# Optimization experiments

Hardware: AMD Instinct MI355X
Metric: run time of the kernel (lower is better)

Reference implementation:

```python
import jax, jax.numpy as jnp
import numpy as np

B, LQ, LK = 4, 256, 512
DQ = DK = PROJ = 256


def setup_inputs() -> dict:
    key = jax.random.key(0)
    ks = jax.random.split(key, 8)
    query = jax.random.normal(ks[0], (B, LQ, DQ), dtype=jnp.float32)
    keys = jax.random.normal(ks[1], (B, LK, DK), dtype=jnp.float32)
    attn_mask = jax.random.bernoulli(ks[2], 0.1, (B, LQ, LK))
    # Linear(query_size+key_size, proj) split into query/key halves (same math as concat @ W1)
    s1 = 1.0 / np.sqrt(DQ + DK)
    Wq = jax.random.uniform(ks[3], (DQ, PROJ), jnp.float32, -s1, s1)
    Wk = jax.random.uniform(ks[4], (DK, PROJ), jnp.float32, -s1, s1)
    b1 = jax.random.uniform(ks[5], (PROJ,), jnp.float32, -s1, s1)
    s2 = 1.0 / np.sqrt(PROJ)
    w2 = jax.random.uniform(ks[6], (PROJ,), jnp.float32, -s2, s2)
    b2 = jax.random.uniform(ks[7], (), jnp.float32, -s2, s2)
    return {"query": query, "keys": keys, "attn_mask": attn_mask,
            "Wq": Wq, "Wk": Wk, "b1": b1, "w2": w2, "b2": b2}


def reference(query, keys, attn_mask, Wq, Wk, b1, w2, b2):
    # cat(q_expand, k_expand) @ W1 == q@Wq broadcast-added to k@Wk (avoids the huge concat)
    qp = jnp.einsum('bqd,dp->bqp', query, Wq)            # (B,Lq,P)
    kp = jnp.einsum('bkd,dp->bkp', keys, Wk)             # (B,Lk,P)
    h = jnp.tanh(qp[:, :, None, :] + kp[:, None, :, :] + b1)  # (B,Lq,Lk,P)
    logits = jnp.einsum('bqkp,p->bqk', h, w2) + b2        # (B,Lq,Lk)
    logits = jnp.where(attn_mask, -jnp.inf, logits)
    return logits
```

## Files before the change

### kernel.cpp

```cpp
#include <hip/hip_runtime.h>
#include <math.h>

#define B_ 4
#define LQ_ 256
#define LK_ 512
#define D_ 256
#define P_ 256

#define SC 2.8853900817779268f

#define MASK_SENTINEL (-3.0e38f)

__global__ __launch_bounds__(128) void proj_kernel(
    const float* __restrict__ Q, const float* __restrict__ Kx,
    const float* __restrict__ Wq, const float* __restrict__ Wk,
    const float* __restrict__ b1,
    float* __restrict__ Eq, float* __restrict__ Ek)
{
    __shared__ __align__(16) float As[64][36];
    __shared__ __align__(16) float Ws[64][68];

    const int bm = blockIdx.x >> 2;
    const int bn = blockIdx.x & 3;
    const bool isq = (bm < 32);
    const int m0 = isq ? bm * 32 : (bm - 32) * 32;
    const float* A = isq ? Q : Kx;
    const float* W = isq ? Wq : Wk;
    float* outp    = isq ? Eq : Ek;
    const int n0 = bn * 64;

    const int t  = threadIdx.x;
    const int tx = t & 15;
    const int ty = t >> 4;

    float acc[4][4] = {};

    for (int kt = 0; kt < 4; ++kt) {
        const int d0 = kt * 64;
        __syncthreads();
        #pragma unroll
        for (int i = 0; i < 4; ++i) {
            int f  = t + i * 128;
            int m  = f >> 4;
            int c4 = (f & 15) * 4;
            float4 v = *(const float4*)&A[(size_t)(m0 + m) * D_ + d0 + c4];
            As[c4 + 0][m] = v.x;
            As[c4 + 1][m] = v.y;
            As[c4 + 2][m] = v.z;
            As[c4 + 3][m] = v.w;
        }
        #pragma unroll
        for (int i = 0; i < 8; ++i) {
            int f  = t + i * 128;
            int r  = f >> 4;
            int c4 = (f & 15) * 4;
            *(float4*)&Ws[r][c4] = *(const float4*)&W[(size_t)(d0 + r) * P_ + n0 + c4];
        }
        __syncthreads();
        #pragma unroll 8
        for (int k = 0; k < 64; ++k) {
            float4 a = *(const float4*)&As[k][ty * 4];
            float4 w = *(const float4*)&Ws[k][tx * 4];
            float av[4] = {a.x, a.y, a.z, a.w};
            float wv[4] = {w.x, w.y, w.z, w.w};
            #pragma unroll
            for (int i = 0; i < 4; ++i)
                #pragma unroll
                for (int j = 0; j < 4; ++j)
                    acc[i][j] = fmaf(av[i], wv[j], acc[i][j]);
        }
    }

    float bv[4] = {0.f, 0.f, 0.f, 0.f};
    if (!isq) {
        float4 b = *(const float4*)&b1[n0 + tx * 4];
        bv[0] = b.x; bv[1] = b.y; bv[2] = b.z; bv[3] = b.w;
    }

    #pragma unroll
    for (int i = 0; i < 4; ++i) {
        int m = m0 + ty * 4 + i;
        float4 o;
        o.x = __builtin_amdgcn_exp2f(SC * (acc[i][0] + bv[0]));
        o.y = __builtin_amdgcn_exp2f(SC * (acc[i][1] + bv[1]));
        o.z = __builtin_amdgcn_exp2f(SC * (acc[i][2] + bv[2]));
        o.w = __builtin_amdgcn_exp2f(SC * (acc[i][3] + bv[3]));
        *(float4*)&outp[(size_t)m * P_ + n0 + tx * 4] = o;
    }
}

__global__ __launch_bounds__(256) void logits_kernel(
    const float* __restrict__ Eq, const float* __restrict__ Ek,
    const unsigned char* __restrict__ mask,
    const float* __restrict__ w2, const float* __restrict__ b2,
    float* __restrict__ out)
{
    __shared__ __align__(16) float eqs[32][260];
    __shared__ __align__(16) float eks[32][260];
    __shared__ __align__(16) float ws2[256];
    __shared__ float partial[4];

    const int b  = blockIdx.z;
    const int q0 = blockIdx.y * 32;
    const int k0 = blockIdx.x * 32;
    const int t  = threadIdx.x;

    #pragma unroll
    for (int i = 0; i < 8; ++i) {
        int f = t + i * 256;
        int r = f >> 6;
        int c = (f & 63) * 4;
        *(float4*)&eqs[r][c] = *(const float4*)&Eq[(size_t)(b * LQ_ + q0 + r) * P_ + c];
        *(float4*)&eks[r][c] = *(const float4*)&Ek[(size_t)(b * LK_ + k0 + r) * P_ + c];
    }
    float wv = w2[t];
    ws2[t] = wv;
    #pragma unroll
    for (int s = 32; s > 0; s >>= 1) wv += __shfl_xor(wv, s);
    if ((t & 63) == 0) partial[t >> 6] = wv;
    __syncthreads();

    const float base = partial[0] + partial[1] + partial[2] + partial[3] + b2[0];

    const int tx = t & 15;
    const int ty = t >> 4;

    size_t oidx[2][2];
    unsigned char mb[2][2];
    #pragma unroll
    for (int i = 0; i < 2; ++i)
        #pragma unroll
        for (int j = 0; j < 2; ++j) {
            oidx[i][j] = (size_t)(b * LQ_ + q0 + ty + i * 16) * LK_ + (k0 + tx + j * 16);
            mb[i][j] = mask[oidx[i][j]];
        }

    const float* q0p = &eqs[ty][0];
    const float* q1p = &eqs[ty + 16][0];
    const float* k0p = &eks[tx][0];
    const float* k1p = &eks[tx + 16][0];

    float acc[2][2] = {};

    #pragma unroll 4
    for (int p4 = 0; p4 < 64; ++p4) {
        float4 qv[2], kv[2], w;
        qv[0] = *(const float4*)(q0p + p4 * 4);
        qv[1] = *(const float4*)(q1p + p4 * 4);
        kv[0] = *(const float4*)(k0p + p4 * 4);
        kv[1] = *(const float4*)(k1p + p4 * 4);
        w     = *(const float4*)&ws2[p4 * 4];
        float qa[2][4] = {{qv[0].x,qv[0].y,qv[0].z,qv[0].w},
                          {qv[1].x,qv[1].y,qv[1].z,qv[1].w}};
        float ka[2][4] = {{kv[0].x,kv[0].y,kv[0].z,kv[0].w},
                          {kv[1].x,kv[1].y,kv[1].z,kv[1].w}};
        #pragma unroll
        for (int i = 0; i < 2; ++i)
            #pragma unroll
            for (int j = 0; j < 2; ++j) {
                float x0 = fmaf(qa[i][0], ka[j][0], 1.f);
                float x1 = fmaf(qa[i][1], ka[j][1], 1.f);
                float x2 = fmaf(qa[i][2], ka[j][2], 1.f);
                float x3 = fmaf(qa[i][3], ka[j][3], 1.f);
                float d01 = x0 * x1;
                float d23 = x2 * x3;
                float n01 = fmaf(w.x, x1, w.y * x0);
                float n23 = fmaf(w.z, x3, w.w * x2);
                float den = d01 * d23;
                float num = fmaf(n01, d23, n23 * d01);
                acc[i][j] = fmaf(num, __builtin_amdgcn_rcpf(den), acc[i][j]);
            }
    }

    #pragma unroll
    for (int i = 0; i < 2; ++i)
        #pragma unroll
        for (int j = 0; j < 2; ++j)
            out[oidx[i][j]] = mb[i][j] ? MASK_SENTINEL : fmaf(-2.f, acc[i][j], base);
}

extern "C" void kernel_launch(void* const* d_in, const int* in_sizes, int n_in,
                              void* d_out, int out_size, void* d_ws, size_t ws_size,
                              hipStream_t stream) {
    const float* query        = (const float*)d_in[0];
    const float* keys         = (const float*)d_in[1];
    const unsigned char* mask = (const unsigned char*)d_in[2];
    const float* Wq           = (const float*)d_in[3];
    const float* Wk           = (const float*)d_in[4];
    const float* b1           = (const float*)d_in[5];
    const float* w2           = (const float*)d_in[6];
    const float* b2           = (const float*)d_in[7];
    float* out = (float*)d_out;

    float* Eq = (float*)d_ws;
    float* Ek = Eq + (size_t)B_ * LQ_ * P_;

    proj_kernel<<<384, 128, 0, stream>>>(query, keys, Wq, Wk, b1, Eq, Ek);

    dim3 g2(LK_ / 32, LQ_ / 32, B_);
    logits_kernel<<<g2, 256, 0, stream>>>(Eq, Ek, mask, w2, b2, out);
}
```

Baseline: 37.54 us.

## Split logits over P into partial tiles with 4x4 register blocking plus combine kernel

The logits kernel now uses 64x64 q/k tiles with a 4x4 per-thread register block and splits the P dimension into four 64-wide chunks across blocks, writing partial sums to a workspace. A new combine kernel sums the four partials, applies bias and mask with vectorized float4 loads and stores, and writes the output. The aim is more reuse of each shared-memory load and a smaller shared-memory footprint per block. The cost is an extra launch plus writing and rereading 4x the output size in partials, and w2 is now read from global memory inside the inner loop.

```diff
diff --git a/kernel.cpp b/kernel.cpp
--- a/kernel.cpp
+++ b/kernel.cpp
@@ -89,75 +89,56 @@
     }
 }
 
-__global__ __launch_bounds__(256) void logits_kernel(
+__global__ __launch_bounds__(256) void logits_partial_kernel(
     const float* __restrict__ Eq, const float* __restrict__ Ek,
-    const unsigned char* __restrict__ mask,
-    const float* __restrict__ w2, const float* __restrict__ b2,
-    float* __restrict__ out)
+    const float* __restrict__ w2, float* __restrict__ part)
 {
-    __shared__ __align__(16) float eqs[32][260];
-    __shared__ __align__(16) float eks[32][260];
-    __shared__ __align__(16) float ws2[256];
-    __shared__ float partial[4];
-
-    const int b  = blockIdx.z;
-    const int q0 = blockIdx.y * 32;
-    const int k0 = blockIdx.x * 32;
+    __shared__ __align__(16) float eqs[64][68];
+    __shared__ __align__(16) float eks[64][68];
+
+    const int kt = blockIdx.x;
+    const int qt = blockIdx.y;
+    const int zz = blockIdx.z;
+    const int b  = zz >> 2;
+    const int pc = zz & 3;
+    const int q0 = qt * 64, k0 = kt * 64, p0 = pc * 64;
     const int t  = threadIdx.x;
-
-    #pragma unroll
-    for (int i = 0; i < 8; ++i) {
-        int f = t + i * 256;
-        int r = f >> 6;
-        int c = (f & 63) * 4;
-        *(float4*)&eqs[r][c] = *(const float4*)&Eq[(size_t)(b * LQ_ + q0 + r) * P_ + c];
-        *(float4*)&eks[r][c] = *(const float4*)&Ek[(size_t)(b * LK_ + k0 + r) * P_ + c];
-    }
-    float wv = w2[t];
-    ws2[t] = wv;
-    #pragma unroll
-    for (int s = 32; s > 0; s >>= 1) wv += __shfl_xor(wv, s);
-    if ((t & 63) == 0) partial[t >> 6] = wv;
-    __syncthreads();
-
-    const float base = partial[0] + partial[1] + partial[2] + partial[3] + b2[0];
-
     const int tx = t & 15;
     const int ty = t >> 4;
 
-    size_t oidx[2][2];
-    unsigned char mb[2][2];
-    #pragma unroll
-    for (int i = 0; i < 2; ++i)
-        #pragma unroll
-        for (int j = 0; j < 2; ++j) {
-            oidx[i][j] = (size_t)(b * LQ_ + q0 + ty + i * 16) * LK_ + (k0 + tx + j * 16);
-            mb[i][j] = mask[oidx[i][j]];
-        }
-
-    const float* q0p = &eqs[ty][0];
-    const float* q1p = &eqs[ty + 16][0];
-    const float* k0p = &eks[tx][0];
-    const float* k1p = &eks[tx + 16][0];
-
-    float acc[2][2] = {};
+    #pragma unroll
+    for (int i = 0; i < 4; ++i) {
+        int f  = t + i * 256;
+        int r  = f >> 4;
+        int c4 = (f & 15) * 4;
+        *(float4*)&eqs[r][c4] = *(const float4*)&Eq[(size_t)(b * LQ_ + q0 + r) * P_ + p0 + c4];
+        *(float4*)&eks[r][c4] = *(const float4*)&Ek[(size_t)(b * LK_ + k0 + r) * P_ + p0 + c4];
+    }
+    __syncthreads();
+
+    float acc[4][4] = {};
 
     #pragma unroll 4
-    for (int p4 = 0; p4 < 64; ++p4) {
-        float4 qv[2], kv[2], w;
-        qv[0] = *(const float4*)(q0p + p4 * 4);
-        qv[1] = *(const float4*)(q1p + p4 * 4);
-        kv[0] = *(const float4*)(k0p + p4 * 4);
-        kv[1] = *(const float4*)(k1p + p4 * 4);
-        w     = *(const float4*)&ws2[p4 * 4];
-        float qa[2][4] = {{qv[0].x,qv[0].y,qv[0].z,qv[0].w},
-                          {qv[1].x,qv[1].y,qv[1].z,qv[1].w}};
-        float ka[2][4] = {{kv[0].x,kv[0].y,kv[0].z,kv[0].w},
-                          {kv[1].x,kv[1].y,kv[1].z,kv[1].w}};
-        #pragma unroll
-        for (int i = 0; i < 2; ++i)
+    for (int p4 = 0; p4 < 16; ++p4) {
+        const float4 w = *(const float4*)&w2[p0 + p4 * 4];
+        float4 qv[4], kv[4];
+        #pragma unroll
+        for (int i = 0; i < 4; ++i) {
+            qv[i] = *(const float4*)&eqs[ty + i * 16][p4 * 4];
+            kv[i] = *(const float4*)&eks[tx + i * 16][p4 * 4];
+        }
+        float qa[4][4] = {{qv[0].x,qv[0].y,qv[0].z,qv[0].w},
+                          {qv[1].x,qv[1].y,qv[1].z,qv[1].w},
+                          {qv[2].x,qv[2].y,qv[2].z,qv[2].w},
+                          {qv[3].x,qv[3].y,qv[3].z,qv[3].w}};
+        float ka[4][4] = {{kv[0].x,kv[0].y,kv[0].z,kv[0].w},
+                          {kv[1].x,kv[1].y,kv[1].z,kv[1].w},
+                          {kv[2].x,kv[2].y,kv[2].z,kv[2].w},
+                          {kv[3].x,kv[3].y,kv[3].z,kv[3].w}};
+        #pragma unroll
+        for (int i = 0; i < 4; ++i)
             #pragma unroll
-            for (int j = 0; j < 2; ++j) {
+            for (int j = 0; j < 4; ++j) {
                 float x0 = fmaf(qa[i][0], ka[j][0], 1.f);
                 float x1 = fmaf(qa[i][1], ka[j][1], 1.f);
                 float x2 = fmaf(qa[i][2], ka[j][2], 1.f);
@@ -166,17 +147,50 @@
                 float d23 = x2 * x3;
                 float n01 = fmaf(w.x, x1, w.y * x0);
                 float n23 = fmaf(w.z, x3, w.w * x2);
-                float den = d01 * d23;
-                float num = fmaf(n01, d23, n23 * d01);
-                acc[i][j] = fmaf(num, __builtin_amdgcn_rcpf(den), acc[i][j]);
+                acc[i][j] = fmaf(fmaf(n01, d23, n23 * d01),
+                                 __builtin_amdgcn_rcpf(d01 * d23),
+                                 acc[i][j]);
             }
     }
 
-    #pragma unroll
-    for (int i = 0; i < 2; ++i)
-        #pragma unroll
-        for (int j = 0; j < 2; ++j)
-            out[oidx[i][j]] = mb[i][j] ? MASK_SENTINEL : fmaf(-2.f, acc[i][j], base);
+    float* pp = part + (size_t)pc * ((size_t)B_ * LQ_ * LK_);
+    #pragma unroll
+    for (int i = 0; i < 4; ++i)
+        #pragma unroll
+        for (int j = 0; j < 4; ++j)
+            pp[(size_t)(b * LQ_ + q0 + ty + i * 16) * LK_ + (k0 + tx + j * 16)] = acc[i][j];
+}
+
+__global__ __launch_bounds__(256) void combine_kernel(
+    const float* __restrict__ part, const unsigned char* __restrict__ mask,
+    const float* __restrict__ w2, const float* __restrict__ b2,
+    float* __restrict__ out)
+{
+    __shared__ float ps[4];
+    const int t = threadIdx.x;
+
+    float wv = w2[t];
+    #pragma unroll
+    for (int s = 32; s > 0; s >>= 1) wv += __shfl_xor(wv, s);
+    if ((t & 63) == 0) ps[t >> 6] = wv;
+    __syncthreads();
+    const float base = ps[0] + ps[1] + ps[2] + ps[3] + b2[0];
+
+    const size_t idx4 = (size_t)blockIdx.x * 256 + t;
+    const size_t STR4 = (size_t)B_ * LQ_ * LK_ / 4;
+
+    const float4 s0 = ((const float4*)part)[idx4];
+    const float4 s1 = ((const float4*)part)[idx4 + STR4];
+    const float4 s2 = ((const float4*)part)[idx4 + 2 * STR4];
+    const float4 s3 = ((const float4*)part)[idx4 + 3 * STR4];
+    const unsigned int mb = ((const unsigned int*)mask)[idx4];
+
+    float4 o;
+    o.x = (mb & 0x000000ffu) ? MASK_SENTINEL : fmaf(-2.f, s0.x + s1.x + s2.x + s3.x, base);
+    o.y = (mb & 0x0000ff00u) ? MASK_SENTINEL : fmaf(-2.f, s0.y + s1.y + s2.y + s3.y, base);
+    o.z = (mb & 0x00ff0000u) ? MASK_SENTINEL : fmaf(-2.f, s0.z + s1.z + s2.z + s3.z, base);
+    o.w = (mb & 0xff000000u) ? MASK_SENTINEL : fmaf(-2.f, s0.w + s1.w + s2.w + s3.w, base);
+    ((float4*)out)[idx4] = o;
 }
 
 extern "C" void kernel_launch(void* const* d_in, const int* in_sizes, int n_in,
@@ -192,11 +206,14 @@
     const float* b2           = (const float*)d_in[7];
     float* out = (float*)d_out;
 
-    float* Eq = (float*)d_ws;
-    float* Ek = Eq + (size_t)B_ * LQ_ * P_;
+    float* Eq   = (float*)d_ws;
+    float* Ek   = Eq + (size_t)B_ * LQ_ * P_;
+    float* part = Ek + (size_t)B_ * LK_ * P_;
 
     proj_kernel<<<384, 128, 0, stream>>>(query, keys, Wq, Wk, b1, Eq, Ek);
 
-    dim3 g2(LK_ / 32, LQ_ / 32, B_);
-    logits_kernel<<<g2, 256, 0, stream>>>(Eq, Ek, mask, w2, b2, out);
-}
+    dim3 g2(LK_ / 64, LQ_ / 64, B_ * 4);
+    logits_partial_kernel<<<g2, 256, 0, stream>>>(Eq, Ek, w2, part);
+
+    combine_kernel<<<512, 256, 0, stream>>>(part, mask, w2, b2, out);
+}
```

Measured after the change: 41.99 us. 1.12x slower.
